# Kernel tuning notes

Hardware: AMD Instinct MI355X
Metric: run time of the kernel (lower is better)

## Reference

```python
import jax, jax.numpy as jnp
import numpy as np

LOG2 = float(np.log(2.0))


def setup_inputs() -> dict:
    key = jax.random.key(0)
    ks = jax.random.split(key, 10)
    V, G, F, T = 262144, 4096, 256, 2
    node_feats = jax.random.normal(ks[0], (V, F), dtype=jnp.float32)
    segment_ids = jnp.sort(jax.random.randint(ks[1], (V,), 0, G))
    s = 0.05
    return {
        "node_feats": node_feats,
        "segment_ids": segment_ids,
        "num_graphs": G,
        "logit_w": jax.random.normal(ks[2], (T, 2 * F, 1), dtype=jnp.float32) * s,
        "logit_b": jnp.zeros((T, 1), dtype=jnp.float32),
        "proj_w": jax.random.normal(ks[3], (T, F, F), dtype=jnp.float32) * s,
        "proj_b": jnp.zeros((T, F), dtype=jnp.float32),
        "gru_w_ih": jax.random.normal(ks[4], (T, 3 * F, F), dtype=jnp.float32) * s,
        "gru_w_hh": jax.random.normal(ks[5], (T, 3 * F, F), dtype=jnp.float32) * s,
        "gru_b_ih": jnp.zeros((T, 3 * F), dtype=jnp.float32),
        "gru_b_hh": jnp.zeros((T, 3 * F), dtype=jnp.float32),
    }


def _gru_cell(x, h, w_ih, w_hh, b_ih, b_hh):
    # torch.nn.GRUCell math
    gi = x @ w_ih.T + b_ih  # [G, 3F]
    gh = h @ w_hh.T + b_hh
    i_r, i_z, i_n = jnp.split(gi, 3, axis=-1)
    h_r, h_z, h_n = jnp.split(gh, 3, axis=-1)
    r = jax.nn.sigmoid(i_r + h_r)
    z = jax.nn.sigmoid(i_z + h_z)
    n = jnp.tanh(i_n + r * h_n)
    return (1.0 - z) * n + z * h


def reference(node_feats, segment_ids, num_graphs, logit_w, logit_b,
              proj_w, proj_b, gru_w_ih, gru_w_hh, gru_b_ih, gru_b_hh):
    G = int(num_graphs)
    # initial graph feats: sum of node feats per graph
    g_feats = jax.ops.segment_sum(node_feats, segment_ids, num_segments=G)
    T = logit_w.shape[0]
    for t in range(T):
        # broadcast relu(g_feats) to nodes, concat with node feats, compute logits
        ctx_nodes = jax.nn.relu(g_feats)[segment_ids]              # [V, F]
        z = jnp.concatenate([ctx_nodes, node_feats], axis=-1) @ logit_w[t] + logit_b[t]  # [V,1]
        z = jnp.logaddexp(z, 0.0) - LOG2                           # SoftPlus2
        # segment softmax over nodes within each graph
        zmax = jax.ops.segment_max(z, segment_ids, num_segments=G)
        e = jnp.exp(z - zmax[segment_ids])
        denom = jax.ops.segment_sum(e, segment_ids, num_segments=G)
        a = e / denom[segment_ids]                                 # [V,1]
        # project nodes (dropout=0) and attention-weighted sum per graph
        hv = node_feats @ proj_w[t] + proj_b[t]                    # [V, F]
        g_repr = jax.ops.segment_sum(a * hv, segment_ids, num_segments=G)
        context = jax.nn.elu(g_repr)
        g_feats = _gru_cell(context, g_feats, gru_w_ih[t], gru_w_hh[t], gru_b_ih[t], gru_b_hh[t])
    return g_feats
```

## Files before the change

kernel.cpp:

```cpp
#include <hip/hip_runtime.h>
#include <hip/hip_bf16.h>
#include <math.h>

#define V_NODES 262144
#define NGRAPH  4096
#define FD      256
#define TSTEPS  2
#define GP      8
#define SB      512
#define RS      264
#define EWCAP   1536

typedef unsigned short u16;
typedef __attribute__((ext_vector_type(8))) short short8;
typedef __attribute__((ext_vector_type(4))) float f32x4;

__device__ __forceinline__ float bf2f(u16 u) {
  union { unsigned int i; float f; } x; x.i = ((unsigned int)u) << 16; return x.f;
}
__device__ __forceinline__ u16 f2bf(float f) {
  union { unsigned int i; float f; } x; x.f = f;
  unsigned int r = x.i + 0x7FFFu + ((x.i >> 16) & 1u);
  return (u16)(r >> 16);
}
__device__ __forceinline__ unsigned int pkbf(float a, float b) {
  return (unsigned int)f2bf(a) | ((unsigned int)f2bf(b) << 16);
}
__device__ __forceinline__ float softplus2(float x) {
  return fmaxf(x, 0.0f) + log1pf(__expf(-fabsf(x))) - 0.69314718056f;
}
__device__ __forceinline__ float dot8(const float4 x0, const float4 x1, const float* w) {
  float d = fmaf(x0.x, w[0], fmaf(x0.y, w[1], fmaf(x0.z, w[2], x0.w * w[3])));
  return fmaf(x1.x, w[4], fmaf(x1.y, w[5], fmaf(x1.z, w[6], fmaf(x1.w, w[7], d))));
}

__global__ __launch_bounds__(256) void k_prep(
    const int* __restrict__ seg, const float* __restrict__ w_ih,
    const float* __restrict__ w_hh, const float* __restrict__ proj_w,
    int* __restrict__ start, u16* __restrict__ wihbf, u16* __restrict__ whhbf,
    u16* __restrict__ whhlo, u16* __restrict__ pwtbf) {
  __shared__ float tl[32][33];
  const int b = blockIdx.x, tid = threadIdx.x;
  const int gtid = b * 256 + tid;
  {
    const int v = gtid;
    const int s = seg[v];
    if (v == 0) {
      for (int g = 0; g <= s; ++g) start[g] = 0;
    } else {
      const int p = seg[v - 1];
      for (int g = p + 1; g <= s; ++g) start[g] = v;
    }
    if (v == V_NODES - 1)
      for (int g = s + 1; g <= NGRAPH; ++g) start[g] = V_NODES;
  }
  {
    const int nchunk = TSTEPS * 768 * FD / 4;
    if (gtid < nchunk) {
      const float4 x = ((const float4*)w_ih)[gtid];
      uint2 u; u.x = pkbf(x.x, x.y); u.y = pkbf(x.z, x.w);
      ((uint2*)wihbf)[gtid] = u;
      const float4 y = ((const float4*)w_hh)[gtid];
      const u16 h0 = f2bf(y.x), h1 = f2bf(y.y), h2 = f2bf(y.z), h3 = f2bf(y.w);
      uint2 hi_, lo_;
      hi_.x = (unsigned)h0 | ((unsigned)h1 << 16);
      hi_.y = (unsigned)h2 | ((unsigned)h3 << 16);
      lo_.x = pkbf(y.x - bf2f(h0), y.y - bf2f(h1));
      lo_.y = pkbf(y.z - bf2f(h2), y.w - bf2f(h3));
      ((uint2*)whhbf)[gtid] = hi_;
      ((uint2*)whhlo)[gtid] = lo_;
    }
  }
  if (b < 2 * 64) {
    const int t = b >> 6, tile = b & 63, bx = tile & 7, by = tile >> 3;
    const int tx = tid & 31, ty = tid >> 5;
    const float* S = proj_w + (size_t)t * FD * FD;
    u16* D = pwtbf + (size_t)t * FD * FD;
#pragma unroll
    for (int i = 0; i < 32; i += 8)
      tl[ty + i][tx] = S[(size_t)(by * 32 + ty + i) * FD + bx * 32 + tx];
    __syncthreads();
#pragma unroll
    for (int i = 0; i < 32; i += 8)
      D[(size_t)(bx * 32 + ty + i) * FD + by * 32 + tx] = f2bf(tl[tx][ty + i]);
  }
}

__global__ __launch_bounds__(SB, 4) void k_main(
    const float* __restrict__ nf, const int* __restrict__ start,
    const float* __restrict__ logit_w, const float* __restrict__ logit_b,
    const float* __restrict__ proj_b, const float* __restrict__ b_ih,
    const float* __restrict__ b_hh, u16* __restrict__ nbf,
    float* __restrict__ gf_out, const u16* __restrict__ wihbf,
    const u16* __restrict__ whhbf, const u16* __restrict__ whhlo,
    const u16* __restrict__ pwtbf) {
  __shared__ __align__(16) float gf_s[GP][FD];
  __shared__ __align__(16) float ew[EWCAP];
  __shared__ __align__(16) float2 dle[EWCAP];
  __shared__ __align__(16) u16 wns_s[16 * RS];
  __shared__ __align__(16) u16 ctx_s[16 * RS];
  __shared__ __align__(16) u16 hhi_s[16 * RS];
  __shared__ __align__(16) u16 hlo_s[16 * RS];

  const int b = blockIdx.x, tid = threadIdx.x;
  const int wv = tid >> 6, lane = tid & 63;
  const int half = lane >> 5, sl = lane & 31;
  const int g0 = b * GP;
  const int g = g0 + wv;
  const int vs = start[g0];
  const int s = start[g], e = start[g + 1];

  for (int i = tid; i < 8 * RS; i += SB) {
    wns_s[8 * RS + i] = 0; ctx_s[8 * RS + i] = 0;
    hhi_s[8 * RS + i] = 0; hlo_s[8 * RS + i] = 0;
  }

  {
    float wA[8], wB[8];
    {
      const float4 a0 = ((const float4*)(logit_w + FD))[2 * sl];
      const float4 a1 = ((const float4*)(logit_w + FD))[2 * sl + 1];
      const float4 b0 = ((const float4*)(logit_w + 512 + FD))[2 * sl];
      const float4 b1 = ((const float4*)(logit_w + 512 + FD))[2 * sl + 1];
      wA[0]=a0.x; wA[1]=a0.y; wA[2]=a0.z; wA[3]=a0.w;
      wA[4]=a1.x; wA[5]=a1.y; wA[6]=a1.z; wA[7]=a1.w;
      wB[0]=b0.x; wB[1]=b0.y; wB[2]=b0.z; wB[3]=b0.w;
      wB[4]=b1.x; wB[5]=b1.y; wB[6]=b1.z; wB[7]=b1.w;
    }
    float ac[8];
#pragma unroll
    for (int j = 0; j < 8; ++j) ac[j] = 0.f;
    const float4* nfv = (const float4*)nf;
    int v = s + half;
    for (; v + 2 < e; v += 4) {
      const float4 x0 = nfv[(size_t)v * 64 + 2 * sl];
      const float4 x1 = nfv[(size_t)v * 64 + 2 * sl + 1];
      const float4 y0 = nfv[(size_t)(v + 2) * 64 + 2 * sl];
      const float4 y1 = nfv[(size_t)(v + 2) * 64 + 2 * sl + 1];
      uint4 u0, u1;
      u0.x = pkbf(x0.x, x0.y); u0.y = pkbf(x0.z, x0.w);
      u0.z = pkbf(x1.x, x1.y); u0.w = pkbf(x1.z, x1.w);
      ((uint4*)(nbf + (size_t)v * FD))[sl] = u0;
      u1.x = pkbf(y0.x, y0.y); u1.y = pkbf(y0.z, y0.w);
      u1.z = pkbf(y1.x, y1.y); u1.w = pkbf(y1.z, y1.w);
      ((uint4*)(nbf + (size_t)(v + 2) * FD))[sl] = u1;
      ac[0] += x0.x + y0.x; ac[1] += x0.y + y0.y;
      ac[2] += x0.z + y0.z; ac[3] += x0.w + y0.w;
      ac[4] += x1.x + y1.x; ac[5] += x1.y + y1.y;
      ac[6] += x1.z + y1.z; ac[7] += x1.w + y1.w;
      float dA0 = dot8(x0, x1, wA), dB0 = dot8(x0, x1, wB);
      float dA1 = dot8(y0, y1, wA), dB1 = dot8(y0, y1, wB);
#pragma unroll
      for (int off = 1; off < 32; off <<= 1) {
        dA0 += __shfl_xor(dA0, off, 64); dB0 += __shfl_xor(dB0, off, 64);
        dA1 += __shfl_xor(dA1, off, 64); dB1 += __shfl_xor(dB1, off, 64);
      }
      if (sl == 0) {
        dle[v - vs] = make_float2(dA0, dB0);
        dle[v + 2 - vs] = make_float2(dA1, dB1);
      }
    }
    if (v < e) {
      const float4 x0 = nfv[(size_t)v * 64 + 2 * sl];
      const float4 x1 = nfv[(size_t)v * 64 + 2 * sl + 1];
      uint4 u0;
      u0.x = pkbf(x0.x, x0.y); u0.y = pkbf(x0.z, x0.w);
      u0.z = pkbf(x1.x, x1.y); u0.w = pkbf(x1.z, x1.w);
      ((uint4*)(nbf + (size_t)v * FD))[sl] = u0;
      ac[0] += x0.x; ac[1] += x0.y; ac[2] += x0.z; ac[3] += x0.w;
      ac[4] += x1.x; ac[5] += x1.y; ac[6] += x1.z; ac[7] += x1.w;
      float dA0 = dot8(x0, x1, wA), dB0 = dot8(x0, x1, wB);
#pragma unroll
      for (int off = 1; off < 32; off <<= 1) {
        dA0 += __shfl_xor(dA0, off, 64); dB0 += __shfl_xor(dB0, off, 64);
      }
      if (sl == 0) dle[v - vs] = make_float2(dA0, dB0);
    }
#pragma unroll
    for (int j = 0; j < 8; ++j) ac[j] += __shfl_xor(ac[j], 32, 64);
    if (half == 0) {
      ((float4*)&gf_s[wv][sl * 8])[0] = make_float4(ac[0], ac[1], ac[2], ac[3]);
      ((float4*)&gf_s[wv][sl * 8])[1] = make_float4(ac[4], ac[5], ac[6], ac[7]);
    }
  }
  __syncthreads();

  for (int t = 0; t < TSTEPS; ++t) {
    for (int i = tid; i < GP * FD; i += SB) {
      const float x = gf_s[i >> 8][i & 255];
      const u16 hb = f2bf(x);
      hhi_s[(i >> 8) * RS + (i & 255)] = hb;
      hlo_s[(i >> 8) * RS + (i & 255)] = f2bf(x - bf2f(hb));
    }
    {
      const float lb = logit_b[t];
      const float4 h4 = ((const float4*)&gf_s[wv][0])[lane];
      const float4 w4 = ((const float4*)(logit_w + (size_t)t * 512))[lane];
      float c = fmaf(fmaxf(h4.x, 0.f), w4.x, fmaf(fmaxf(h4.y, 0.f), w4.y,
                fmaf(fmaxf(h4.z, 0.f), w4.z, fmaxf(h4.w, 0.f) * w4.w)));
#pragma unroll
      for (int off = 1; off < 64; off <<= 1) c += __shfl_xor(c, off, 64);
      float m = -1e30f;
      for (int v2 = s + lane; v2 < e; v2 += 64) {
        const float2 dd = dle[v2 - vs];
        const float z = softplus2(c + (t ? dd.y : dd.x) + lb);
        ew[v2 - vs] = z;
        m = fmaxf(m, z);
      }
#pragma unroll
      for (int off = 1; off < 64; off <<= 1) m = fmaxf(m, __shfl_xor(m, off, 64));
      float ls = 0.f;
      for (int v2 = s + lane; v2 < e; v2 += 64) {
        const float ez = __expf(ew[v2 - vs] - m);
        ew[v2 - vs] = ez;
        ls += ez;
      }
#pragma unroll
      for (int off = 1; off < 64; off <<= 1) ls += __shfl_xor(ls, off, 64);
      const float inv = (e > s) ? 1.0f / ls : 0.f;
      for (int v2 = s + lane; v2 < e; v2 += 64) ew[v2 - vs] *= inv;
      float acc[8];
#pragma unroll
      for (int j = 0; j < 8; ++j) acc[j] = 0.f;
      int v = s + half;
      for (; v + 2 < e; v += 4) {
        const uint4 u0 = ((const uint4*)(nbf + (size_t)v * FD))[sl];
        const uint4 u1 = ((const uint4*)(nbf + (size_t)(v + 2) * FD))[sl];
        const float a0 = ew[v - vs], a1 = ew[v + 2 - vs];
        acc[0] = fmaf(a0, bf2f((u16)(u0.x & 0xffff)), acc[0]);
        acc[1] = fmaf(a0, bf2f((u16)(u0.x >> 16)),    acc[1]);
        acc[2] = fmaf(a0, bf2f((u16)(u0.y & 0xffff)), acc[2]);
        acc[3] = fmaf(a0, bf2f((u16)(u0.y >> 16)),    acc[3]);
        acc[4] = fmaf(a0, bf2f((u16)(u0.z & 0xffff)), acc[4]);
        acc[5] = fmaf(a0, bf2f((u16)(u0.z >> 16)),    acc[5]);
        acc[6] = fmaf(a0, bf2f((u16)(u0.w & 0xffff)), acc[6]);
        acc[7] = fmaf(a0, bf2f((u16)(u0.w >> 16)),    acc[7]);
        acc[0] = fmaf(a1, bf2f((u16)(u1.x & 0xffff)), acc[0]);
        acc[1] = fmaf(a1, bf2f((u16)(u1.x >> 16)),    acc[1]);
        acc[2] = fmaf(a1, bf2f((u16)(u1.y & 0xffff)), acc[2]);
        acc[3] = fmaf(a1, bf2f((u16)(u1.y >> 16)),    acc[3]);
        acc[4] = fmaf(a1, bf2f((u16)(u1.z & 0xffff)), acc[4]);
        acc[5] = fmaf(a1, bf2f((u16)(u1.z >> 16)),    acc[5]);
        acc[6] = fmaf(a1, bf2f((u16)(u1.w & 0xffff)), acc[6]);
        acc[7] = fmaf(a1, bf2f((u16)(u1.w >> 16)),    acc[7]);
      }
      if (v < e) {
        const uint4 u0 = ((const uint4*)(nbf + (size_t)v * FD))[sl];
        const float a0 = ew[v - vs];
        acc[0] = fmaf(a0, bf2f((u16)(u0.x & 0xffff)), acc[0]);
        acc[1] = fmaf(a0, bf2f((u16)(u0.x >> 16)),    acc[1]);
        acc[2] = fmaf(a0, bf2f((u16)(u0.y & 0xffff)), acc[2]);
        acc[3] = fmaf(a0, bf2f((u16)(u0.y >> 16)),    acc[3]);
        acc[4] = fmaf(a0, bf2f((u16)(u0.z & 0xffff)), acc[4]);
        acc[5] = fmaf(a0, bf2f((u16)(u0.z >> 16)),    acc[5]);
        acc[6] = fmaf(a0, bf2f((u16)(u0.w & 0xffff)), acc[6]);
        acc[7] = fmaf(a0, bf2f((u16)(u0.w >> 16)),    acc[7]);
      }
#pragma unroll
      for (int j = 0; j < 8; ++j) acc[j] += __shfl_xor(acc[j], 32, 64);
      if (half == 0) {
        uint4 w;
        w.x = pkbf(acc[0], acc[1]); w.y = pkbf(acc[2], acc[3]);
        w.z = pkbf(acc[4], acc[5]); w.w = pkbf(acc[6], acc[7]);
        *(uint4*)(wns_s + wv * RS + sl * 8) = w;
      }
    }
    __syncthreads();
    {
      const int r = lane & 15, q = lane >> 4;
      const u16* xp = wns_s + r * RS + q * 8;
#pragma unroll
      for (int jj = 0; jj < 2; ++jj) {
        const int nt = wv * 2 + jj;
        const u16* wp = pwtbf + (size_t)t * FD * FD + (size_t)(nt * 16 + r) * FD + q * 8;
        f32x4 a4 = {0.f, 0.f, 0.f, 0.f};
#pragma unroll
        for (int kt = 0; kt < 8; ++kt) {
          const short8 av = *(const short8*)(xp + kt * 32);
          const short8 bv = *(const short8*)(wp + kt * 32);
          a4 = __builtin_amdgcn_mfma_f32_16x16x32_bf16(av, bv, a4, 0, 0, 0);
        }
        const int gcol = nt * 16 + r;
        const float bs = proj_b[t * FD + gcol];
#pragma unroll
        for (int i = 0; i < 4; ++i) {
          float vv = a4[i] + bs;
          vv = (vv > 0.0f) ? vv : expm1f(vv);
          ctx_s[(q * 4 + i) * RS + gcol] = f2bf(vv);
        }
      }
    }
    __syncthreads();
    {
      const int r = lane & 15, q = lane >> 4;
      const u16* xi = ctx_s + r * RS + q * 8;
      const u16* xh = hhi_s + r * RS + q * 8;
      const u16* xl = hlo_s + r * RS + q * 8;
      const u16* wih_t = wihbf + (size_t)t * 768 * FD;
      const u16* whh_t = whhbf + (size_t)t * 768 * FD;
      const u16* whl_t = whhlo + (size_t)t * 768 * FD;
      auto gpair = [&](const u16* wi, const u16* wh, const u16* wl,
                       f32x4& ai, f32x4& ah) {
#pragma unroll
        for (int kt = 0; kt < 8; ++kt) {
          const short8 aiv = *(const short8*)(xi + kt * 32);
          const short8 bi  = *(const short8*)(wi + kt * 32);
          ai = __builtin_amdgcn_mfma_f32_16x16x32_bf16(aiv, bi, ai, 0, 0, 0);
          const short8 xhh = *(const short8*)(xh + kt * 32);
          const short8 xll = *(const short8*)(xl + kt * 32);
          const short8 bh  = *(const short8*)(wh + kt * 32);
          const short8 bl  = *(const short8*)(wl + kt * 32);
          ah = __builtin_amdgcn_mfma_f32_16x16x32_bf16(xhh, bh, ah, 0, 0, 0);
          ah = __builtin_amdgcn_mfma_f32_16x16x32_bf16(xll, bh, ah, 0, 0, 0);
          ah = __builtin_amdgcn_mfma_f32_16x16x32_bf16(xhh, bl, ah, 0, 0, 0);
        }
      };
#pragma unroll
      for (int jj = 0; jj < 2; ++jj) {
        const int col = (wv * 2 + jj) * 16 + r;
        float rr[4], zz[4];
        {
          f32x4 ai = {0.f,0.f,0.f,0.f}, ah = {0.f,0.f,0.f,0.f};
          gpair(wih_t + (size_t)col * FD + q * 8,
                whh_t + (size_t)col * FD + q * 8,
                whl_t + (size_t)col * FD + q * 8, ai, ah);
          const float bi_ = b_ih[t * 768 + col], bh_ = b_hh[t * 768 + col];
#pragma unroll
          for (int i = 0; i < 4; ++i)
            rr[i] = 1.f / (1.f + __expf(-(ai[i] + bi_ + ah[i] + bh_)));
        }
        {
          f32x4 ai = {0.f,0.f,0.f,0.f}, ah = {0.f,0.f,0.f,0.f};
          gpair(wih_t + (size_t)(256 + col) * FD + q * 8,
                whh_t + (size_t)(256 + col) * FD + q * 8,
                whl_t + (size_t)(256 + col) * FD + q * 8, ai, ah);
          const float bi_ = b_ih[t * 768 + 256 + col], bh_ = b_hh[t * 768 + 256 + col];
#pragma unroll
          for (int i = 0; i < 4; ++i)
            zz[i] = 1.f / (1.f + __expf(-(ai[i] + bi_ + ah[i] + bh_)));
        }
        {
          f32x4 ai = {0.f,0.f,0.f,0.f}, ah = {0.f,0.f,0.f,0.f};
          gpair(wih_t + (size_t)(512 + col) * FD + q * 8,
                whh_t + (size_t)(512 + col) * FD + q * 8,
                whl_t + (size_t)(512 + col) * FD + q * 8, ai, ah);
          const float bi_ = b_ih[t * 768 + 512 + col], bh_ = b_hh[t * 768 + 512 + col];
          if (q < 2) {
#pragma unroll
            for (int i = 0; i < 4; ++i) {
              const int row = q * 4 + i;
              const float nn = tanhf(ai[i] + bi_ + rr[i] * (ah[i] + bh_));
              const float hold = gf_s[row][col];
              gf_s[row][col] = (1.f - zz[i]) * nn + zz[i] * hold;
            }
          }
        }
      }
    }
    __syncthreads();
  }

  ((float4*)(gf_out + (size_t)g0 * FD))[tid] = ((const float4*)gf_s)[tid];
}

extern "C" void kernel_launch(void* const* d_in, const int* in_sizes, int n_in,
                              void* d_out, int out_size, void* d_ws, size_t ws_size,
                              hipStream_t stream) {
  const float* node    = (const float*)d_in[0];
  const int*   seg     = (const int*)d_in[1];
  const float* logit_w = (const float*)d_in[3];
  const float* logit_b = (const float*)d_in[4];
  const float* proj_w  = (const float*)d_in[5];
  const float* proj_b  = (const float*)d_in[6];
  const float* w_ih    = (const float*)d_in[7];
  const float* w_hh    = (const float*)d_in[8];
  const float* b_ih    = (const float*)d_in[9];
  const float* b_hh    = (const float*)d_in[10];
  float* gfeats = (float*)d_out;

  char* p = (char*)d_ws;
  int* start   = (int*)p;   p += (((NGRAPH + 1) * sizeof(int)) + 255) & ~(size_t)255;
  u16* nbf     = (u16*)p;   p += (size_t)V_NODES * FD * 2;
  u16* wihbf   = (u16*)p;   p += (size_t)TSTEPS * 768 * FD * 2;
  u16* whhbf   = (u16*)p;   p += (size_t)TSTEPS * 768 * FD * 2;
  u16* whhlo   = (u16*)p;   p += (size_t)TSTEPS * 768 * FD * 2;
  u16* pwtbf   = (u16*)p;   p += (size_t)TSTEPS * FD * FD * 2;
  (void)ws_size; (void)in_sizes; (void)n_in; (void)out_size;

  k_prep<<<dim3(V_NODES / 256), dim3(256), 0, stream>>>(
      seg, w_ih, w_hh, proj_w, start, wihbf, whhbf, whhlo, pwtbf);
  k_main<<<dim3(NGRAPH / GP), dim3(SB), 0, stream>>>(
      node, start, logit_w, logit_b, proj_b, b_ih, b_hh, nbf, gfeats,
      wihbf, whhbf, whhlo, pwtbf);
}
```

Baseline: 658.1 us.

## Split node streaming pass into separate per-graph kernel before step kernel

```diff
diff --git a/kernel.cpp b/kernel.cpp
--- a/kernel.cpp
+++ b/kernel.cpp
@@ -86,17 +86,93 @@
   }
 }
 
-__global__ __launch_bounds__(SB, 4) void k_main(
+__global__ __launch_bounds__(256) void k_pass1(
     const float* __restrict__ nf, const int* __restrict__ start,
-    const float* __restrict__ logit_w, const float* __restrict__ logit_b,
-    const float* __restrict__ proj_b, const float* __restrict__ b_ih,
-    const float* __restrict__ b_hh, u16* __restrict__ nbf,
-    float* __restrict__ gf_out, const u16* __restrict__ wihbf,
-    const u16* __restrict__ whhbf, const u16* __restrict__ whhlo,
-    const u16* __restrict__ pwtbf) {
+    const float* __restrict__ logit_w, float* __restrict__ gf,
+    u16* __restrict__ nbf, float* __restrict__ d0, float* __restrict__ d1) {
+  __shared__ __align__(16) float redf[8][FD];
+  const int g = blockIdx.x, tid = threadIdx.x;
+  const int h = tid >> 5, sl = tid & 31;
+  const int s = start[g], e = start[g + 1];
+  float wA[8], wB[8];
+  {
+    const float4 a0 = ((const float4*)(logit_w + FD))[2 * sl];
+    const float4 a1 = ((const float4*)(logit_w + FD))[2 * sl + 1];
+    const float4 b0 = ((const float4*)(logit_w + 512 + FD))[2 * sl];
+    const float4 b1 = ((const float4*)(logit_w + 512 + FD))[2 * sl + 1];
+    wA[0]=a0.x; wA[1]=a0.y; wA[2]=a0.z; wA[3]=a0.w;
+    wA[4]=a1.x; wA[5]=a1.y; wA[6]=a1.z; wA[7]=a1.w;
+    wB[0]=b0.x; wB[1]=b0.y; wB[2]=b0.z; wB[3]=b0.w;
+    wB[4]=b1.x; wB[5]=b1.y; wB[6]=b1.z; wB[7]=b1.w;
+  }
+  float ac[8];
+#pragma unroll
+  for (int j = 0; j < 8; ++j) ac[j] = 0.f;
+  const float4* nfv = (const float4*)nf;
+  int v = s + h;
+  for (; v + 8 < e; v += 16) {
+    const float4 x0 = nfv[(size_t)v * 64 + 2 * sl];
+    const float4 x1 = nfv[(size_t)v * 64 + 2 * sl + 1];
+    const float4 y0 = nfv[(size_t)(v + 8) * 64 + 2 * sl];
+    const float4 y1 = nfv[(size_t)(v + 8) * 64 + 2 * sl + 1];
+    uint4 u0, u1;
+    u0.x = pkbf(x0.x, x0.y); u0.y = pkbf(x0.z, x0.w);
+    u0.z = pkbf(x1.x, x1.y); u0.w = pkbf(x1.z, x1.w);
+    ((uint4*)(nbf + (size_t)v * FD))[sl] = u0;
+    u1.x = pkbf(y0.x, y0.y); u1.y = pkbf(y0.z, y0.w);
+    u1.z = pkbf(y1.x, y1.y); u1.w = pkbf(y1.z, y1.w);
+    ((uint4*)(nbf + (size_t)(v + 8) * FD))[sl] = u1;
+    ac[0] += x0.x + y0.x; ac[1] += x0.y + y0.y;
+    ac[2] += x0.z + y0.z; ac[3] += x0.w + y0.w;
+    ac[4] += x1.x + y1.x; ac[5] += x1.y + y1.y;
+    ac[6] += x1.z + y1.z; ac[7] += x1.w + y1.w;
+    float dA0 = dot8(x0, x1, wA), dB0 = dot8(x0, x1, wB);
+    float dA1 = dot8(y0, y1, wA), dB1 = dot8(y0, y1, wB);
+#pragma unroll
+    for (int off = 1; off < 32; off <<= 1) {
+      dA0 += __shfl_xor(dA0, off, 64); dB0 += __shfl_xor(dB0, off, 64);
+      dA1 += __shfl_xor(dA1, off, 64); dB1 += __shfl_xor(dB1, off, 64);
+    }
+    if (sl == 0) {
+      d0[v] = dA0; d1[v] = dB0;
+      d0[v + 8] = dA1; d1[v + 8] = dB1;
+    }
+  }
+  for (; v < e; v += 8) {
+    const float4 x0 = nfv[(size_t)v * 64 + 2 * sl];
+    const float4 x1 = nfv[(size_t)v * 64 + 2 * sl + 1];
+    uint4 u0;
+    u0.x = pkbf(x0.x, x0.y); u0.y = pkbf(x0.z, x0.w);
+    u0.z = pkbf(x1.x, x1.y); u0.w = pkbf(x1.z, x1.w);
+    ((uint4*)(nbf + (size_t)v * FD))[sl] = u0;
+    ac[0] += x0.x; ac[1] += x0.y; ac[2] += x0.z; ac[3] += x0.w;
+    ac[4] += x1.x; ac[5] += x1.y; ac[6] += x1.z; ac[7] += x1.w;
+    float dA0 = dot8(x0, x1, wA), dB0 = dot8(x0, x1, wB);
+#pragma unroll
+    for (int off = 1; off < 32; off <<= 1) {
+      dA0 += __shfl_xor(dA0, off, 64); dB0 += __shfl_xor(dB0, off, 64);
+    }
+    if (sl == 0) { d0[v] = dA0; d1[v] = dB0; }
+  }
+  ((float4*)&redf[h][sl * 8])[0] = make_float4(ac[0], ac[1], ac[2], ac[3]);
+  ((float4*)&redf[h][sl * 8])[1] = make_float4(ac[4], ac[5], ac[6], ac[7]);
+  __syncthreads();
+  float sum = 0.f;
+#pragma unroll
+  for (int j = 0; j < 8; ++j) sum += redf[j][tid];
+  gf[(size_t)g * FD + tid] = sum;
+}
+
+__global__ __launch_bounds__(SB, 4) void k_steps(
+    const int* __restrict__ start, const float* __restrict__ logit_w,
+    const float* __restrict__ logit_b, const float* __restrict__ proj_b,
+    const float* __restrict__ b_ih, const float* __restrict__ b_hh,
+    const u16* __restrict__ nbf, const float* __restrict__ d0,
+    const float* __restrict__ d1, float* __restrict__ gf_out,
+    const u16* __restrict__ wihbf, const u16* __restrict__ whhbf,
+    const u16* __restrict__ whhlo, const u16* __restrict__ pwtbf) {
   __shared__ __align__(16) float gf_s[GP][FD];
   __shared__ __align__(16) float ew[EWCAP];
-  __shared__ __align__(16) float2 dle[EWCAP];
   __shared__ __align__(16) u16 wns_s[16 * RS];
   __shared__ __align__(16) u16 ctx_s[16 * RS];
   __shared__ __align__(16) u16 hhi_s[16 * RS];
@@ -111,78 +187,11 @@
   const int s = start[g], e = start[g + 1];
 
   for (int i = tid; i < 8 * RS; i += SB) {
-    wns_s[8 * RS + i] = 0; ctx_s[8 * RS + i] = 0;
+    wns_s[8 * RS + i] = 0;
     hhi_s[8 * RS + i] = 0; hlo_s[8 * RS + i] = 0;
   }
-
-  {
-    float wA[8], wB[8];
-    {
-      const float4 a0 = ((const float4*)(logit_w + FD))[2 * sl];
-      const float4 a1 = ((const float4*)(logit_w + FD))[2 * sl + 1];
-      const float4 b0 = ((const float4*)(logit_w + 512 + FD))[2 * sl];
-      const float4 b1 = ((const float4*)(logit_w + 512 + FD))[2 * sl + 1];
-      wA[0]=a0.x; wA[1]=a0.y; wA[2]=a0.z; wA[3]=a0.w;
-      wA[4]=a1.x; wA[5]=a1.y; wA[6]=a1.z; wA[7]=a1.w;
-      wB[0]=b0.x; wB[1]=b0.y; wB[2]=b0.z; wB[3]=b0.w;
-      wB[4]=b1.x; wB[5]=b1.y; wB[6]=b1.z; wB[7]=b1.w;
-    }
-    float ac[8];
-#pragma unroll
-    for (int j = 0; j < 8; ++j) ac[j] = 0.f;
-    const float4* nfv = (const float4*)nf;
-    int v = s + half;
-    for (; v + 2 < e; v += 4) {
-      const float4 x0 = nfv[(size_t)v * 64 + 2 * sl];
-      const float4 x1 = nfv[(size_t)v * 64 + 2 * sl + 1];
-      const float4 y0 = nfv[(size_t)(v + 2) * 64 + 2 * sl];
-      const float4 y1 = nfv[(size_t)(v + 2) * 64 + 2 * sl + 1];
-      uint4 u0, u1;
-      u0.x = pkbf(x0.x, x0.y); u0.y = pkbf(x0.z, x0.w);
-      u0.z = pkbf(x1.x, x1.y); u0.w = pkbf(x1.z, x1.w);
-      ((uint4*)(nbf + (size_t)v * FD))[sl] = u0;
-      u1.x = pkbf(y0.x, y0.y); u1.y = pkbf(y0.z, y0.w);
-      u1.z = pkbf(y1.x, y1.y); u1.w = pkbf(y1.z, y1.w);
-      ((uint4*)(nbf + (size_t)(v + 2) * FD))[sl] = u1;
-      ac[0] += x0.x + y0.x; ac[1] += x0.y + y0.y;
-      ac[2] += x0.z + y0.z; ac[3] += x0.w + y0.w;
-      ac[4] += x1.x + y1.x; ac[5] += x1.y + y1.y;
-      ac[6] += x1.z + y1.z; ac[7] += x1.w + y1.w;
-      float dA0 = dot8(x0, x1, wA), dB0 = dot8(x0, x1, wB);
-      float dA1 = dot8(y0, y1, wA), dB1 = dot8(y0, y1, wB);
-#pragma unroll
-      for (int off = 1; off < 32; off <<= 1) {
-        dA0 += __shfl_xor(dA0, off, 64); dB0 += __shfl_xor(dB0, off, 64);
-        dA1 += __shfl_xor(dA1, off, 64); dB1 += __shfl_xor(dB1, off, 64);
-      }
-      if (sl == 0) {
-        dle[v - vs] = make_float2(dA0, dB0);
-        dle[v + 2 - vs] = make_float2(dA1, dB1);
-      }
-    }
-    if (v < e) {
-      const float4 x0 = nfv[(size_t)v * 64 + 2 * sl];
-      const float4 x1 = nfv[(size_t)v * 64 + 2 * sl + 1];
-      uint4 u0;
-      u0.x = pkbf(x0.x, x0.y); u0.y = pkbf(x0.z, x0.w);
-      u0.z = pkbf(x1.x, x1.y); u0.w = pkbf(x1.z, x1.w);
-      ((uint4*)(nbf + (size_t)v * FD))[sl] = u0;
-      ac[0] += x0.x; ac[1] += x0.y; ac[2] += x0.z; ac[3] += x0.w;
-      ac[4] += x1.x; ac[5] += x1.y; ac[6] += x1.z; ac[7] += x1.w;
-      float dA0 = dot8(x0, x1, wA), dB0 = dot8(x0, x1, wB);
-#pragma unroll
-      for (int off = 1; off < 32; off <<= 1) {
-        dA0 += __shfl_xor(dA0, off, 64); dB0 += __shfl_xor(dB0, off, 64);
-      }
-      if (sl == 0) dle[v - vs] = make_float2(dA0, dB0);
-    }
-#pragma unroll
-    for (int j = 0; j < 8; ++j) ac[j] += __shfl_xor(ac[j], 32, 64);
-    if (half == 0) {
-      ((float4*)&gf_s[wv][sl * 8])[0] = make_float4(ac[0], ac[1], ac[2], ac[3]);
-      ((float4*)&gf_s[wv][sl * 8])[1] = make_float4(ac[4], ac[5], ac[6], ac[7]);
-    }
-  }
+  for (int i = tid; i < GP * FD; i += SB)
+    gf_s[i >> 8][i & 255] = gf_out[(size_t)g0 * FD + i];
   __syncthreads();
 
   for (int t = 0; t < TSTEPS; ++t) {
@@ -194,6 +203,7 @@
     }
     {
       const float lb = logit_b[t];
+      const float* dt = t ? d1 : d0;
       const float4 h4 = ((const float4*)&gf_s[wv][0])[lane];
       const float4 w4 = ((const float4*)(logit_w + (size_t)t * 512))[lane];
       float c = fmaf(fmaxf(h4.x, 0.f), w4.x, fmaf(fmaxf(h4.y, 0.f), w4.y,
@@ -202,8 +212,7 @@
       for (int off = 1; off < 64; off <<= 1) c += __shfl_xor(c, off, 64);
       float m = -1e30f;
       for (int v2 = s + lane; v2 < e; v2 += 64) {
-        const float2 dd = dle[v2 - vs];
-        const float z = softplus2(c + (t ? dd.y : dd.x) + lb);
+        const float z = softplus2(c + dt[v2] + lb);
         ew[v2 - vs] = z;
         m = fmaxf(m, z);
       }
@@ -223,10 +232,13 @@
 #pragma unroll
       for (int j = 0; j < 8; ++j) acc[j] = 0.f;
       int v = s + half;
-      for (; v + 2 < e; v += 4) {
+      for (; v + 6 < e; v += 8) {
         const uint4 u0 = ((const uint4*)(nbf + (size_t)v * FD))[sl];
         const uint4 u1 = ((const uint4*)(nbf + (size_t)(v + 2) * FD))[sl];
+        const uint4 u2 = ((const uint4*)(nbf + (size_t)(v + 4) * FD))[sl];
+        const uint4 u3 = ((const uint4*)(nbf + (size_t)(v + 6) * FD))[sl];
         const float a0 = ew[v - vs], a1 = ew[v + 2 - vs];
+        const float a2 = ew[v + 4 - vs], a3 = ew[v + 6 - vs];
         acc[0] = fmaf(a0, bf2f((u16)(u0.x & 0xffff)), acc[0]);
         acc[1] = fmaf(a0, bf2f((u16)(u0.x >> 16)),    acc[1]);
         acc[2] = fmaf(a0, bf2f((u16)(u0.y & 0xffff)), acc[2]);
@@ -243,8 +255,24 @@
         acc[5] = fmaf(a1, bf2f((u16)(u1.z >> 16)),    acc[5]);
         acc[6] = fmaf(a1, bf2f((u16)(u1.w & 0xffff)), acc[6]);
         acc[7] = fmaf(a1, bf2f((u16)(u1.w >> 16)),    acc[7]);
-      }
-      if (v < e) {
+        acc[0] = fmaf(a2, bf2f((u16)(u2.x & 0xffff)), acc[0]);
+        acc[1] = fmaf(a2, bf2f((u16)(u2.x >> 16)),    acc[1]);
+        acc[2] = fmaf(a2, bf2f((u16)(u2.y & 0xffff)), acc[2]);
+        acc[3] = fmaf(a2, bf2f((u16)(u2.y >> 16)),    acc[3]);
+        acc[4] = fmaf(a2, bf2f((u16)(u2.z & 0xffff)), acc[4]);
+        acc[5] = fmaf(a2, bf2f((u16)(u2.z >> 16)),    acc[5]);
+        acc[6] = fmaf(a2, bf2f((u16)(u2.w & 0xffff)), acc[6]);
+        acc[7] = fmaf(a2, bf2f((u16)(u2.w >> 16)),    acc[7]);
+        acc[0] = fmaf(a3, bf2f((u16)(u3.x & 0xffff)), acc[0]);
+        acc[1] = fmaf(a3, bf2f((u16)(u3.x >> 16)),    acc[1]);
+        acc[2] = fmaf(a3, bf2f((u16)(u3.y & 0xffff)), acc[2]);
+        acc[3] = fmaf(a3, bf2f((u16)(u3.y >> 16)),    acc[3]);
+        acc[4] = fmaf(a3, bf2f((u16)(u3.z & 0xffff)), acc[4]);
+        acc[5] = fmaf(a3, bf2f((u16)(u3.z >> 16)),    acc[5]);
+        acc[6] = fmaf(a3, bf2f((u16)(u3.w & 0xffff)), acc[6]);
+        acc[7] = fmaf(a3, bf2f((u16)(u3.w >> 16)),    acc[7]);
+      }
+      for (; v < e; v += 2) {
         const uint4 u0 = ((const uint4*)(nbf + (size_t)v * FD))[sl];
         const float a0 = ew[v - vs];
         acc[0] = fmaf(a0, bf2f((u16)(u0.x & 0xffff)), acc[0]);
@@ -381,6 +409,8 @@
   char* p = (char*)d_ws;
   int* start   = (int*)p;   p += (((NGRAPH + 1) * sizeof(int)) + 255) & ~(size_t)255;
   u16* nbf     = (u16*)p;   p += (size_t)V_NODES * FD * 2;
+  float* d0    = (float*)p; p += (size_t)V_NODES * 4;
+  float* d1    = (float*)p; p += (size_t)V_NODES * 4;
   u16* wihbf   = (u16*)p;   p += (size_t)TSTEPS * 768 * FD * 2;
   u16* whhbf   = (u16*)p;   p += (size_t)TSTEPS * 768 * FD * 2;
   u16* whhlo   = (u16*)p;   p += (size_t)TSTEPS * 768 * FD * 2;
@@ -389,7 +419,9 @@
 
   k_prep<<<dim3(V_NODES / 256), dim3(256), 0, stream>>>(
       seg, w_ih, w_hh, proj_w, start, wihbf, whhbf, whhlo, pwtbf);
-  k_main<<<dim3(NGRAPH / GP), dim3(SB), 0, stream>>>(
-      node, start, logit_w, logit_b, proj_b, b_ih, b_hh, nbf, gfeats,
-      wihbf, whhbf, whhlo, pwtbf);
-}
+  k_pass1<<<dim3(NGRAPH), dim3(256), 0, stream>>>(
+      node, start, logit_w, gfeats, nbf, d0, d1);
+  k_steps<<<dim3(NGRAPH / GP), dim3(SB), 0, stream>>>(
+      start, logit_w, logit_b, proj_b, b_ih, b_hh, nbf, d0, d1,
+      gfeats, wihbf, whhbf, whhlo, pwtbf);
+}
```

Result: slower. 681.4 us (+3.5%).
